# Optimization experiments

Hardware: AMD Instinct MI355X
Metric: run time of the kernel (lower is better)

## Reference

```python
import jax, jax.numpy as jnp
import numpy as np

D_MODEL = 1024
N_HEADS = 16
HEAD_DIM = D_MODEL // N_HEADS


def setup_inputs() -> dict:
    key = jax.random.key(0)
    ks = jax.random.split(key, 6)
    B, S = 4, 2048
    query = jax.random.normal(ks[0], (B, S, D_MODEL), dtype=jnp.float32)
    key_value = jax.random.normal(ks[1], (B, S, D_MODEL), dtype=jnp.float32)
    scale = 1.0 / np.sqrt(D_MODEL)
    Wq = jax.random.normal(ks[2], (D_MODEL, D_MODEL), dtype=jnp.float32) * scale
    Wk = jax.random.normal(ks[3], (D_MODEL, D_MODEL), dtype=jnp.float32) * scale
    Wv = jax.random.normal(ks[4], (D_MODEL, D_MODEL), dtype=jnp.float32) * scale
    Wo = jax.random.normal(ks[5], (D_MODEL, D_MODEL), dtype=jnp.float32) * scale
    return {"query": query, "key_value": key_value, "Wq": Wq, "Wk": Wk, "Wv": Wv, "Wo": Wo}


def reference(query, key_value, Wq, Wk, Wv, Wo):
    B, S, _ = query.shape
    H, Dh = N_HEADS, HEAD_DIM
    # nn.Linear (no bias): y = x @ W.T ; then split heads -> [B, H, S, Dh]
    q = (query @ Wq.T).reshape(B, S, H, Dh).transpose(0, 2, 1, 3)
    k = (key_value @ Wk.T).reshape(B, S, H, Dh).transpose(0, 2, 1, 3)
    v = (key_value @ Wv.T).reshape(B, S, H, Dh).transpose(0, 2, 1, 3)
    scale = Dh ** -0.5
    scores = jnp.einsum("bhqd,bhkd->bhqk", q, k) * scale  # [B,H,S,S]
    causal = jnp.tril(jnp.ones((S, S), dtype=bool))  # True where allowed
    scores = jnp.where(causal, scores, -jnp.inf)
    attn = jax.nn.softmax(scores, axis=-1)
    out = jnp.einsum("bhqk,bhkd->bhqd", attn, v)  # [B,H,S,Dh]
    out = out.transpose(0, 2, 1, 3).reshape(B, S, H * Dh)
    return out @ Wo.T
```

## Files before the change

### kernel.cpp

```cpp
#include <hip/hip_runtime.h>
#include <stdint.h>

typedef unsigned short u16;
typedef __attribute__((ext_vector_type(4))) unsigned short u16x4;
typedef __attribute__((ext_vector_type(8))) unsigned short u16x8;
typedef __attribute__((ext_vector_type(8))) __bf16 bf16x8;
typedef __attribute__((ext_vector_type(2))) _Float16 half2;
typedef __attribute__((ext_vector_type(8))) _Float16 half8;
typedef __attribute__((ext_vector_type(4))) float f32x4;

#define SEQ 2048
#define DM 1024
#define NH 16
#define DH 64
#define BATCH 4
#define MROWS (BATCH * SEQ)

#define SC_LOG2E 0.18033688011112042f

__device__ __forceinline__ u16 f2bf(float f) {
    uint32_t u = __builtin_bit_cast(uint32_t, f);
    u += 0x7fffu + ((u >> 16) & 1u);
    return (u16)(u >> 16);
}
__device__ __forceinline__ u16 f2h(float f) {
    return __builtin_bit_cast(u16, (_Float16)f);
}
__device__ __forceinline__ half2 pkrtz(float a, float b) {
    return __builtin_bit_cast(half2, __builtin_amdgcn_cvt_pkrtz(a, b));
}

__device__ __forceinline__ void load16_lds(const void* g, void* l) {
    __builtin_amdgcn_global_load_lds(
        (const __attribute__((address_space(1))) uint32_t*)(uintptr_t)g,
        (__attribute__((address_space(3))) uint32_t*)(uintptr_t)l,
        16, 0, 0);
}

#define N4A (MROWS * DM / 4)
#define N4W (DM * DM / 4)

__device__ __forceinline__ void cvt_one(const float* src, u16* dst, int i) {
    float4 v = ((const float4*)src)[i];
    u16x4 o;
    o[0] = f2bf(v.x); o[1] = f2bf(v.y); o[2] = f2bf(v.z); o[3] = f2bf(v.w);
    *(u16x4*)(dst + (size_t)i * 4) = o;
}

__global__ void cvt_all(const float* __restrict__ q, const float* __restrict__ kv,
                        const float* __restrict__ w0, const float* __restrict__ w1,
                        const float* __restrict__ w2, const float* __restrict__ w3,
                        u16* __restrict__ dq, u16* __restrict__ dkv,
                        u16* __restrict__ dw0, u16* __restrict__ dw1,
                        u16* __restrict__ dw2, u16* __restrict__ dw3) {
    int i = blockIdx.x * 256 + threadIdx.x;
    if (i < N4A) { cvt_one(q, dq, i); return; }
    i -= N4A;
    if (i < N4A) { cvt_one(kv, dkv, i); return; }
    i -= N4A;
    int s = i >> 18;
    int l = i & (N4W - 1);
    const float* src = s == 0 ? w0 : s == 1 ? w1 : s == 2 ? w2 : w3;
    u16* dst = s == 0 ? dw0 : s == 1 ? dw1 : s == 2 ? dw2 : dw3;
    cvt_one(src, dst, l);
}

__global__ __launch_bounds__(256) void qkv_gemm(const u16* __restrict__ q_bf,
                                                const u16* __restrict__ kv_bf,
                                                const u16* __restrict__ wq,
                                                const u16* __restrict__ wk,
                                                const u16* __restrict__ wv,
                                                u16* __restrict__ Qh,
                                                u16* __restrict__ Kh,
                                                u16* __restrict__ Vt) {
    __shared__ __align__(16) u16 lA[128 * 32];
    __shared__ __align__(16) u16 lB[128 * 32];
    const int t = threadIdx.x;
    const int lane = t & 63;
    const int w = t >> 6;
    const int ln = lane & 15, quad = lane >> 4;
    const int sel = blockIdx.x >> 3;
    const int n0 = (blockIdx.x & 7) * 128;
    const int m0 = blockIdx.y * 128;
    const int wm = (w >> 1) * 64, wn = (w & 1) * 64;
    const u16* A = (sel == 0) ? q_bf : kv_bf;
    const u16* B = (sel == 0) ? wq : (sel == 1 ? wk : wv);

    f32x4 acc[4][4] = {};

    for (int k0 = 0; k0 < DM; k0 += 32) {
#pragma unroll
        for (int i = 0; i < 2; ++i) {
            int c = i * 256 + t;
            int row = c >> 2, colq = c & 3;
            load16_lds(A + (size_t)(m0 + row) * DM + k0 + colq * 8, &lA[c * 8]);
            load16_lds(B + (size_t)(n0 + row) * DM + k0 + colq * 8, &lB[c * 8]);
        }
        __syncthreads();

        bf16x8 af[4], bfr[4];
#pragma unroll
        for (int mi = 0; mi < 4; ++mi)
            af[mi] = __builtin_bit_cast(bf16x8, *(const u16x8*)&lA[(wm + mi * 16 + ln) * 32 + quad * 8]);
#pragma unroll
        for (int ni = 0; ni < 4; ++ni)
            bfr[ni] = __builtin_bit_cast(bf16x8, *(const u16x8*)&lB[(wn + ni * 16 + ln) * 32 + quad * 8]);
#pragma unroll
        for (int mi = 0; mi < 4; ++mi)
#pragma unroll
            for (int ni = 0; ni < 4; ++ni)
                acc[mi][ni] = __builtin_amdgcn_mfma_f32_16x16x32_bf16(af[mi], bfr[ni], acc[mi][ni], 0, 0, 0);
        __syncthreads();
    }

    if (sel == 2) {
#pragma unroll
        for (int mi = 0; mi < 4; ++mi) {
            int rowb = m0 + wm + mi * 16 + quad * 4;
            int bb = rowb >> 11, s = rowb & 2047;
#pragma unroll
            for (int ni = 0; ni < 4; ++ni) {
                int col = n0 + wn + ni * 16 + ln;
                int h = col >> 6, d = col & 63;
                u16x4 o;
#pragma unroll
                for (int r = 0; r < 4; ++r) o[r] = f2h(acc[mi][ni][r]);
                *(u16x4*)(Vt + ((size_t)(bb * NH + h) * DH + d) * SEQ + s) = o;
            }
        }
    } else {
        u16* C = sel ? Kh : Qh;
        const float scale = sel ? 1.0f : SC_LOG2E;
#pragma unroll
        for (int mi = 0; mi < 4; ++mi) {
            int rowb = m0 + wm + mi * 16 + quad * 4;
#pragma unroll
            for (int ni = 0; ni < 4; ++ni) {
                int col = n0 + wn + ni * 16 + ln;
                int h = col >> 6, d = col & 63;
#pragma unroll
                for (int r = 0; r < 4; ++r) {
                    int row = rowb + r;
                    int bb = row >> 11, s = row & 2047;
                    C[((size_t)((bb * NH + h) * SEQ + s) << 6) + d] = f2bf(acc[mi][ni][r] * scale);
                }
            }
        }
    }
}

__global__ __launch_bounds__(256) void wo_gemm(const u16* __restrict__ A,
                                               const u16* __restrict__ B,
                                               float* __restrict__ Cout) {
    __shared__ __align__(16) u16 lA[128 * 32];
    __shared__ __align__(16) u16 lB[128 * 32];
    const int t = threadIdx.x;
    const int lane = t & 63;
    const int w = t >> 6;
    const int ln = lane & 15, quad = lane >> 4;
    const int m0 = blockIdx.y * 128, n0 = blockIdx.x * 128;
    const int wm = (w >> 1) * 64, wn = (w & 1) * 64;

    f32x4 acc[4][4] = {};

    for (int k0 = 0; k0 < DM; k0 += 32) {
#pragma unroll
        for (int i = 0; i < 2; ++i) {
            int c = i * 256 + t;
            int row = c >> 2, colq = c & 3;
            load16_lds(A + (size_t)(m0 + row) * DM + k0 + colq * 8, &lA[c * 8]);
            load16_lds(B + (size_t)(n0 + row) * DM + k0 + colq * 8, &lB[c * 8]);
        }
        __syncthreads();

        bf16x8 af[4], bfr[4];
#pragma unroll
        for (int mi = 0; mi < 4; ++mi)
            af[mi] = __builtin_bit_cast(bf16x8, *(const u16x8*)&lA[(wm + mi * 16 + ln) * 32 + quad * 8]);
#pragma unroll
        for (int ni = 0; ni < 4; ++ni)
            bfr[ni] = __builtin_bit_cast(bf16x8, *(const u16x8*)&lB[(wn + ni * 16 + ln) * 32 + quad * 8]);
#pragma unroll
        for (int mi = 0; mi < 4; ++mi)
#pragma unroll
            for (int ni = 0; ni < 4; ++ni)
                acc[mi][ni] = __builtin_amdgcn_mfma_f32_16x16x32_bf16(af[mi], bfr[ni], acc[mi][ni], 0, 0, 0);
        __syncthreads();
    }

#pragma unroll
    for (int mi = 0; mi < 4; ++mi) {
        int rowb = m0 + wm + mi * 16 + quad * 4;
#pragma unroll
        for (int ni = 0; ni < 4; ++ni) {
            int col = n0 + wn + ni * 16 + ln;
#pragma unroll
            for (int r = 0; r < 4; ++r)
                Cout[(size_t)(rowb + r) * DM + col] = acc[mi][ni][r];
        }
    }
}

__global__ __launch_bounds__(256) void attn_kernel(const u16* __restrict__ Q,
                                                   const u16* __restrict__ K,
                                                   const u16* __restrict__ Vt,
                                                   u16* __restrict__ AO) {
    __shared__ __align__(16) u16 qs[128 * 64];
    __shared__ __align__(16) u16 ks[64 * 64];
    __shared__ __align__(16) u16 vs[80 * 64];

    const int t = threadIdx.x;
    const int lane = t & 63, w = t >> 6;
    const int ln = lane & 15, quad = lane >> 4;
    const int l3 = ln & 7;
    const int bi = blockIdx.x;
    const int bh = bi & 63;
    const int qraw = bi >> 6;
    const int qtile = (bh & 1) ? (15 - qraw) : qraw;
    const int q0 = qtile * 128;
    const int qw0 = q0 + w * 32;
    const int ktmax = 2 * qtile + 1;
    const u16* Qb = Q + (size_t)bh * SEQ * DH;
    const u16* Kb = K + (size_t)bh * SEQ * DH;
    const u16* Vb = Vt + (size_t)bh * DH * SEQ;
    const int b = bh >> 4, h = bh & 15;

    const int cb = t & 7;
    const int r0 = t >> 3;
    const int swc = ((cb ^ (r0 & 7)) << 3);
    const int sg = ((r0 & 12) << 1) | ((r0 & 16) >> 2) | (r0 & 3);

    if (t < 128) {
        int j = t >> 3;
        u16 hv = (j == 0) ? 0x3C00 : 0;
        u16x8 o = {hv, hv, hv, hv, hv, hv, hv, hv};
        *(u16x8*)&vs[((64 + j) << 6) | (((t & 7) ^ (j & 7)) << 3)] = o;
    }

    u16x8 qreg[4];
#pragma unroll
    for (int i = 0; i < 4; ++i)
        qreg[i] = *(const u16x8*)(Qb + (size_t)(q0 + r0 + i * 32) * DH + cb * 8);
    u16x8 kreg[2], vreg[2];
#pragma unroll
    for (int i = 0; i < 2; ++i) {
        kreg[i] = *(const u16x8*)(Kb + (size_t)(i * 32 + sg) * DH + cb * 8);
        vreg[i] = *(const u16x8*)(Vb + (size_t)(r0 + i * 32) * SEQ + cb * 8);
    }

    f32x4 oaccT[2][5] = {};

    for (int kt = 0; kt <= ktmax; ++kt) {
        const int kv0 = kt * 64;
        __syncthreads();
        if (kt == 0) {
#pragma unroll
            for (int i = 0; i < 4; ++i)
                *(u16x8*)&qs[((r0 + i * 32) << 6) | swc] = qreg[i];
        }
#pragma unroll
        for (int i = 0; i < 2; ++i) {
            *(u16x8*)&ks[((r0 + i * 32) << 6) | swc] = kreg[i];
            *(u16x8*)&vs[((r0 + i * 32) << 6) | swc] = vreg[i];
        }
        __syncthreads();
        if (kt < ktmax) {
            const int kvn = kv0 + 64;
#pragma unroll
            for (int i = 0; i < 2; ++i) {
                kreg[i] = *(const u16x8*)(Kb + (size_t)(kvn + i * 32 + sg) * DH + cb * 8);
                vreg[i] = *(const u16x8*)(Vb + (size_t)(r0 + i * 32) * SEQ + kvn + cb * 8);
            }
        }

        if (kv0 >= qw0 + 32) continue;

        f32x4 st[2][4] = {};
#pragma unroll
        for (int half = 0; half < 2; ++half) {
            const int swz = (((half * 4 + quad) ^ l3) << 3);
            bf16x8 qf0 = __builtin_bit_cast(bf16x8, *(const u16x8*)&qs[((w * 32 + ln) << 6) | swz]);
            bf16x8 qf1 = __builtin_bit_cast(bf16x8, *(const u16x8*)&qs[((w * 32 + 16 + ln) << 6) | swz]);
#pragma unroll
            for (int ms = 0; ms < 4; ++ms) {
                bf16x8 kf = __builtin_bit_cast(bf16x8, *(const u16x8*)&ks[((ms * 16 + ln) << 6) | swz]);
                st[0][ms] = __builtin_amdgcn_mfma_f32_16x16x32_bf16(kf, qf0, st[0][ms], 0, 0, 0);
                st[1][ms] = __builtin_amdgcn_mfma_f32_16x16x32_bf16(kf, qf1, st[1][ms], 0, 0, 0);
            }
        }

        half8 pf[2][2];
#pragma unroll
        for (int qt2 = 0; qt2 < 2; ++qt2) {
            const int qbase = qw0 + qt2 * 16;
            if (kv0 + 63 > qbase) {
                const int relq = qbase + ln - kv0 - quad * 8;
#pragma unroll
                for (int ms = 0; ms < 4; ++ms)
#pragma unroll
                    for (int r = 0; r < 4; ++r)
                        if ((ms >> 1) * 32 + (ms & 1) * 4 + r > relq)
                            st[qt2][ms][r] = -3e38f;
            }
#pragma unroll
            for (int c = 0; c < 2; ++c) {
                half2 p0 = pkrtz(__builtin_amdgcn_exp2f(st[qt2][2 * c][0]),
                                 __builtin_amdgcn_exp2f(st[qt2][2 * c][1]));
                half2 p1 = pkrtz(__builtin_amdgcn_exp2f(st[qt2][2 * c][2]),
                                 __builtin_amdgcn_exp2f(st[qt2][2 * c][3]));
                half2 p2 = pkrtz(__builtin_amdgcn_exp2f(st[qt2][2 * c + 1][0]),
                                 __builtin_amdgcn_exp2f(st[qt2][2 * c + 1][1]));
                half2 p3 = pkrtz(__builtin_amdgcn_exp2f(st[qt2][2 * c + 1][2]),
                                 __builtin_amdgcn_exp2f(st[qt2][2 * c + 1][3]));
                half8 v;
                v[0] = p0[0]; v[1] = p0[1]; v[2] = p1[0]; v[3] = p1[1];
                v[4] = p2[0]; v[5] = p2[1]; v[6] = p3[0]; v[7] = p3[1];
                pf[qt2][c] = v;
            }
        }

#pragma unroll
        for (int c = 0; c < 2; ++c) {
            const int off = (((c * 4 + quad) ^ l3) << 3);
#pragma unroll
            for (int nd = 0; nd < 5; ++nd) {
                half8 vf = __builtin_bit_cast(half8, *(const u16x8*)&vs[((nd * 16 + ln) << 6) | off]);
                oaccT[0][nd] = __builtin_amdgcn_mfma_f32_16x16x32_f16(vf, pf[0][c], oaccT[0][nd], 0, 0, 0);
                oaccT[1][nd] = __builtin_amdgcn_mfma_f32_16x16x32_f16(vf, pf[1][c], oaccT[1][nd], 0, 0, 0);
            }
        }
    }

#pragma unroll
    for (int qt2 = 0; qt2 < 2; ++qt2) {
        float lv = __shfl(oaccT[qt2][4][0], ln, 64);
        float linv = 1.0f / lv;
        int q = q0 + w * 32 + qt2 * 16 + ln;
        size_t base = ((size_t)(b * SEQ + q) * DM) + h * DH + quad * 4;
#pragma unroll
        for (int nd = 0; nd < 4; ++nd) {
            u16x4 o;
#pragma unroll
            for (int r = 0; r < 4; ++r) o[r] = f2bf(oaccT[qt2][nd][r] * linv);
            *(u16x4*)&AO[base + nd * 16] = o;
        }
    }
}

extern "C" void kernel_launch(void* const* d_in, const int* in_sizes, int n_in,
                              void* d_out, int out_size, void* d_ws, size_t ws_size,
                              hipStream_t stream) {
    const float* query = (const float*)d_in[0];
    const float* key_value = (const float*)d_in[1];
    const float* Wq = (const float*)d_in[2];
    const float* Wk = (const float*)d_in[3];
    const float* Wv = (const float*)d_in[4];
    const float* Wo = (const float*)d_in[5];
    float* out = (float*)d_out;

    char* ws = (char*)d_ws;
    const size_t SZ_ACT = (size_t)MROWS * DM * 2;
    const size_t SZ_W = (size_t)DM * DM * 2;
    u16* q_bf  = (u16*)(ws + 0);
    u16* kv_bf = (u16*)(ws + SZ_ACT);
    u16* wq_bf = (u16*)(ws + 2 * SZ_ACT);
    u16* wk_bf = (u16*)(ws + 2 * SZ_ACT + SZ_W);
    u16* wv_bf = (u16*)(ws + 2 * SZ_ACT + 2 * SZ_W);
    u16* wo_bf = (u16*)(ws + 2 * SZ_ACT + 3 * SZ_W);
    u16* Qh    = (u16*)(ws + 2 * SZ_ACT + 4 * SZ_W);
    u16* Kh    = (u16*)(ws + 2 * SZ_ACT + 4 * SZ_W + SZ_ACT);
    u16* Vt    = (u16*)(ws + 2 * SZ_ACT + 4 * SZ_W + 2 * SZ_ACT);
    u16* AOb   = q_bf;

    const int n4_total = 2 * N4A + 4 * N4W;
    cvt_all<<<n4_total / 256, 256, 0, stream>>>(query, key_value, Wq, Wk, Wv, Wo,
                                                q_bf, kv_bf, wq_bf, wk_bf, wv_bf, wo_bf);

    qkv_gemm<<<dim3(24, MROWS / 128), 256, 0, stream>>>(q_bf, kv_bf, wq_bf, wk_bf, wv_bf,
                                                        Qh, Kh, Vt);

    attn_kernel<<<1024, 256, 0, stream>>>(Qh, Kh, Vt, AOb);

    wo_gemm<<<dim3(DM / 128, MROWS / 128), 256, 0, stream>>>(AOb, wo_bf, out);
}
```

Before: 282.5 us.

## Share a double-buffered swizzled GEMM core across QKV and output projections

Replaces the single-buffered 128x128 GEMM loops with a shared core that uses 512-thread blocks computing 256x128 tiles. It double-buffers LDS across 64-wide K tiles, prefetching the next half-tile while MFMAs run, and XOR-swizzles LDS columns to cut bank conflicts. It also uses setprio and sched barriers around the MFMA block. The aim is to hide global-load latency and raise MFMA utilisation, at the cost of more LDS (96KB per block) and fewer blocks in flight. The hand-written waitcnt and barrier sequencing is easy to get subtly wrong.

New measurement: 272.4 us. 1.04x faster.

```diff
diff --git a/kernel.cpp b/kernel.cpp
--- a/kernel.cpp
+++ b/kernel.cpp
@@ -15,6 +15,7 @@
 #define DH 64
 #define BATCH 4
 #define MROWS (BATCH * SEQ)
+#define NKT 16
 
 #define SC_LOG2E 0.18033688011112042f
 
@@ -65,62 +66,114 @@
     cvt_one(src, dst, l);
 }
 
-__global__ __launch_bounds__(256) void qkv_gemm(const u16* __restrict__ q_bf,
-                                                const u16* __restrict__ kv_bf,
-                                                const u16* __restrict__ wq,
-                                                const u16* __restrict__ wk,
-                                                const u16* __restrict__ wv,
-                                                u16* __restrict__ Qh,
-                                                u16* __restrict__ Kh,
-                                                u16* __restrict__ Vt) {
-    __shared__ __align__(16) u16 lA[128 * 32];
-    __shared__ __align__(16) u16 lB[128 * 32];
+#define LDS_DB 24576
+#define LDS_AH 8192
+#define LDS_BH 4096
+
+__device__ __forceinline__ void gemm_core(const u16* __restrict__ Ag,
+                                          const u16* __restrict__ Bg,
+                                          int m0, int n0, f32x4 (&acc)[4][4]) {
+    __shared__ __align__(16) u16 lds[2 * LDS_DB];
     const int t = threadIdx.x;
     const int lane = t & 63;
     const int w = t >> 6;
     const int ln = lane & 15, quad = lane >> 4;
+    const int wml = (w >> 1) * 64;
+    const int wnl = (w & 1) * 64;
+    const int rowT = t >> 2;
+    const int cswz8 = (((t & 3) ^ ((t >> 3) & 3)) << 3);
+    const int swz = ((quad ^ ((ln >> 1) & 3)) << 3);
+
+    auto stageA = [&](int kt, int h, int d) {
+        const u16* s = Ag + (size_t)(m0 + rowT) * DM + kt * 64 + h * 32 + cswz8;
+        u16* l = &lds[d * LDS_DB + h * LDS_AH + t * 8];
+        load16_lds(s, l);
+        load16_lds(s + (size_t)128 * DM, l + 4096);
+    };
+    auto stageB = [&](int kt, int h, int d) {
+        load16_lds(Bg + (size_t)(n0 + rowT) * DM + kt * 64 + h * 32 + cswz8,
+                   &lds[d * LDS_DB + 2 * LDS_AH + h * LDS_BH + t * 8]);
+    };
+
+    stageA(0, 0, 0); stageB(0, 0, 0);
+    stageA(0, 1, 0); stageB(0, 1, 0);
+    stageA(1, 0, 1); stageB(1, 0, 1);
+    asm volatile("s_waitcnt vmcnt(6)" ::: "memory");
+    __builtin_amdgcn_s_barrier();
+
+    for (int kt = 0; kt < NKT; ++kt) {
+        const int d = kt & 1;
+#pragma unroll
+        for (int h = 0; h < 2; ++h) {
+            const u16* As = &lds[d * LDS_DB + h * LDS_AH];
+            const u16* Bs = &lds[d * LDS_DB + 2 * LDS_AH + h * LDS_BH];
+            bf16x8 af[4], bfr[4];
+#pragma unroll
+            for (int mi = 0; mi < 4; ++mi)
+                af[mi] = __builtin_bit_cast(bf16x8,
+                    *(const u16x8*)&As[(wml + mi * 16 + ln) * 32 + swz]);
+#pragma unroll
+            for (int ni = 0; ni < 4; ++ni)
+                bfr[ni] = __builtin_bit_cast(bf16x8,
+                    *(const u16x8*)&Bs[(wnl + ni * 16 + ln) * 32 + swz]);
+
+            if (h == 0) {
+                int k1 = kt + 1 < NKT ? kt + 1 : NKT - 1;
+                stageA(k1, 1, d ^ 1); stageB(k1, 1, d ^ 1);
+            } else {
+                int k2 = kt + 2 < NKT ? kt + 2 : NKT - 1;
+                stageA(k2, 0, d); stageB(k2, 0, d);
+            }
+
+            __builtin_amdgcn_s_barrier();
+            asm volatile("s_waitcnt lgkmcnt(0)" ::: "memory");
+            __builtin_amdgcn_sched_barrier(0);
+            __builtin_amdgcn_s_setprio(1);
+#pragma unroll
+            for (int mi = 0; mi < 4; ++mi)
+#pragma unroll
+                for (int ni = 0; ni < 4; ++ni)
+                    acc[mi][ni] = __builtin_amdgcn_mfma_f32_16x16x32_bf16(
+                        af[mi], bfr[ni], acc[mi][ni], 0, 0, 0);
+            __builtin_amdgcn_s_setprio(0);
+            __builtin_amdgcn_sched_barrier(0);
+            asm volatile("s_waitcnt vmcnt(6)" ::: "memory");
+            __builtin_amdgcn_s_barrier();
+        }
+    }
+    asm volatile("s_waitcnt vmcnt(0)" ::: "memory");
+}
+
+__global__ __launch_bounds__(512, 2) void qkv_gemm(const u16* __restrict__ q_bf,
+                                                   const u16* __restrict__ kv_bf,
+                                                   const u16* __restrict__ wq,
+                                                   const u16* __restrict__ wk,
+                                                   const u16* __restrict__ wv,
+                                                   u16* __restrict__ Qh,
+                                                   u16* __restrict__ Kh,
+                                                   u16* __restrict__ Vt) {
     const int sel = blockIdx.x >> 3;
     const int n0 = (blockIdx.x & 7) * 128;
-    const int m0 = blockIdx.y * 128;
-    const int wm = (w >> 1) * 64, wn = (w & 1) * 64;
+    const int m0 = blockIdx.y * 256;
     const u16* A = (sel == 0) ? q_bf : kv_bf;
     const u16* B = (sel == 0) ? wq : (sel == 1 ? wk : wv);
 
     f32x4 acc[4][4] = {};
-
-    for (int k0 = 0; k0 < DM; k0 += 32) {
-#pragma unroll
-        for (int i = 0; i < 2; ++i) {
-            int c = i * 256 + t;
-            int row = c >> 2, colq = c & 3;
-            load16_lds(A + (size_t)(m0 + row) * DM + k0 + colq * 8, &lA[c * 8]);
-            load16_lds(B + (size_t)(n0 + row) * DM + k0 + colq * 8, &lB[c * 8]);
-        }
-        __syncthreads();
-
-        bf16x8 af[4], bfr[4];
-#pragma unroll
-        for (int mi = 0; mi < 4; ++mi)
-            af[mi] = __builtin_bit_cast(bf16x8, *(const u16x8*)&lA[(wm + mi * 16 + ln) * 32 + quad * 8]);
-#pragma unroll
-        for (int ni = 0; ni < 4; ++ni)
-            bfr[ni] = __builtin_bit_cast(bf16x8, *(const u16x8*)&lB[(wn + ni * 16 + ln) * 32 + quad * 8]);
-#pragma unroll
-        for (int mi = 0; mi < 4; ++mi)
-#pragma unroll
-            for (int ni = 0; ni < 4; ++ni)
-                acc[mi][ni] = __builtin_amdgcn_mfma_f32_16x16x32_bf16(af[mi], bfr[ni], acc[mi][ni], 0, 0, 0);
-        __syncthreads();
-    }
+    gemm_core(A, B, m0, n0, acc);
+
+    const int t = threadIdx.x;
+    const int lane = t & 63, w = t >> 6;
+    const int ln = lane & 15, quad = lane >> 4;
+    const int wml = (w >> 1) * 64, wnl = (w & 1) * 64;
 
     if (sel == 2) {
 #pragma unroll
         for (int mi = 0; mi < 4; ++mi) {
-            int rowb = m0 + wm + mi * 16 + quad * 4;
+            int rowb = m0 + wml + mi * 16 + quad * 4;
             int bb = rowb >> 11, s = rowb & 2047;
 #pragma unroll
             for (int ni = 0; ni < 4; ++ni) {
-                int col = n0 + wn + ni * 16 + ln;
+                int col = n0 + wnl + ni * 16 + ln;
                 int h = col >> 6, d = col & 63;
                 u16x4 o;
 #pragma unroll
@@ -133,10 +186,10 @@
         const float scale = sel ? 1.0f : SC_LOG2E;
 #pragma unroll
         for (int mi = 0; mi < 4; ++mi) {
-            int rowb = m0 + wm + mi * 16 + quad * 4;
+            int rowb = m0 + wml + mi * 16 + quad * 4;
 #pragma unroll
             for (int ni = 0; ni < 4; ++ni) {
-                int col = n0 + wn + ni * 16 + ln;
+                int col = n0 + wnl + ni * 16 + ln;
                 int h = col >> 6, d = col & 63;
 #pragma unroll
                 for (int r = 0; r < 4; ++r) {
@@ -149,51 +202,25 @@
     }
 }
 
-__global__ __launch_bounds__(256) void wo_gemm(const u16* __restrict__ A,
-                                               const u16* __restrict__ B,
-                                               float* __restrict__ Cout) {
-    __shared__ __align__(16) u16 lA[128 * 32];
-    __shared__ __align__(16) u16 lB[128 * 32];
+__global__ __launch_bounds__(512, 2) void wo_gemm(const u16* __restrict__ A,
+                                                  const u16* __restrict__ B,
+                                                  float* __restrict__ Cout) {
+    const int m0 = blockIdx.y * 256, n0 = blockIdx.x * 128;
+
+    f32x4 acc[4][4] = {};
+    gemm_core(A, B, m0, n0, acc);
+
     const int t = threadIdx.x;
-    const int lane = t & 63;
-    const int w = t >> 6;
+    const int lane = t & 63, w = t >> 6;
     const int ln = lane & 15, quad = lane >> 4;
-    const int m0 = blockIdx.y * 128, n0 = blockIdx.x * 128;
-    const int wm = (w >> 1) * 64, wn = (w & 1) * 64;
-
-    f32x4 acc[4][4] = {};
-
-    for (int k0 = 0; k0 < DM; k0 += 32) {
-#pragma unroll
-        for (int i = 0; i < 2; ++i) {
-            int c = i * 256 + t;
-            int row = c >> 2, colq = c & 3;
-            load16_lds(A + (size_t)(m0 + row) * DM + k0 + colq * 8, &lA[c * 8]);
-            load16_lds(B + (size_t)(n0 + row) * DM + k0 + colq * 8, &lB[c * 8]);
-        }
-        __syncthreads();
-
-        bf16x8 af[4], bfr[4];
-#pragma unroll
-        for (int mi = 0; mi < 4; ++mi)
-            af[mi] = __builtin_bit_cast(bf16x8, *(const u16x8*)&lA[(wm + mi * 16 + ln) * 32 + quad * 8]);
-#pragma unroll
-        for (int ni = 0; ni < 4; ++ni)
-            bfr[ni] = __builtin_bit_cast(bf16x8, *(const u16x8*)&lB[(wn + ni * 16 + ln) * 32 + quad * 8]);
-#pragma unroll
-        for (int mi = 0; mi < 4; ++mi)
-#pragma unroll
-            for (int ni = 0; ni < 4; ++ni)
-                acc[mi][ni] = __builtin_amdgcn_mfma_f32_16x16x32_bf16(af[mi], bfr[ni], acc[mi][ni], 0, 0, 0);
-        __syncthreads();
-    }
+    const int wml = (w >> 1) * 64, wnl = (w & 1) * 64;
 
 #pragma unroll
     for (int mi = 0; mi < 4; ++mi) {
-        int rowb = m0 + wm + mi * 16 + quad * 4;
+        int rowb = m0 + wml + mi * 16 + quad * 4;
 #pragma unroll
         for (int ni = 0; ni < 4; ++ni) {
-            int col = n0 + wn + ni * 16 + ln;
+            int col = n0 + wnl + ni * 16 + ln;
 #pragma unroll
             for (int r = 0; r < 4; ++r)
                 Cout[(size_t)(rowb + r) * DM + col] = acc[mi][ni][r];
@@ -376,10 +403,10 @@
     cvt_all<<<n4_total / 256, 256, 0, stream>>>(query, key_value, Wq, Wk, Wv, Wo,
                                                 q_bf, kv_bf, wq_bf, wk_bf, wv_bf, wo_bf);
 
-    qkv_gemm<<<dim3(24, MROWS / 128), 256, 0, stream>>>(q_bf, kv_bf, wq_bf, wk_bf, wv_bf,
+    qkv_gemm<<<dim3(24, MROWS / 256), 512, 0, stream>>>(q_bf, kv_bf, wq_bf, wk_bf, wv_bf,
                                                         Qh, Kh, Vt);
 
     attn_kernel<<<1024, 256, 0, stream>>>(Qh, Kh, Vt, AOb);
 
-    wo_gemm<<<dim3(DM / 128, MROWS / 128), 256, 0, stream>>>(AOb, wo_bf, out);
-}
+    wo_gemm<<<dim3(DM / 128, MROWS / 256), 512, 0, stream>>>(AOb, wo_bf, out);
+}
```
